# Kernel optimization log

Hardware: AMD Instinct MI355X
Metric: run time of the kernel (lower is better)

The kernel has to match this reference:

```python
import jax, jax.numpy as jnp
import numpy as np

B, S, IN, E, L, H, NC, NL = 4, 1000, 5, 256, 6, 8, 2, 50
DH = E // H


def _ln(x, g, b, eps=1e-5):
    m = jnp.mean(x, -1, keepdims=True)
    v = jnp.mean((x - m) ** 2, -1, keepdims=True)
    return (x - m) / jnp.sqrt(v + eps) * g + b


def _lin(x, w, b):
    return x @ w.T + b


def _ph_single(points, fw, db, law, lab):
    # points: (S, 2) -> (6,) persistence features
    scores = (points @ law.T + lab)[:, 0]
    wts = jax.nn.softmax(scores)
    _, idx = jax.lax.top_k(wts, NL)
    lm = points[idx]  # (NL, 2) landmarks
    d2 = jnp.sum((lm[:, None, :] - lm[None, :, :]) ** 2, -1)
    # safe sqrt (zero grad on zero diagonal) == torch.cdist
    dist = jnp.sqrt(jnp.where(d2 > 0, d2, 1.0)) * (d2 > 0)
    sd = dist * jnp.abs(fw[0, 0]) + db[0]
    K = jnp.exp(-sd)
    lap = jnp.diag(jnp.sum(K, 1)) - K
    ev, evec = jnp.linalg.eigh(lap)
    zm = (ev < 1e-6).astype(ev.dtype)
    n0 = jnp.sum(zm)
    s0 = jnp.sum(jnp.abs(ev) * zm)
    gap = ev[1] - ev[0]
    fied = jnp.std(evec[:, 1], ddof=1)  # torch.std is unbiased
    return jnp.stack([n0, s0, gap, fied, jnp.mean(ev[2:6]), jnp.std(ev[2:6], ddof=1)])


def _attn(x, pf, qw, qb, kw, kb, vw, vb, pw1, pb1, pw2, pb2, ow_, ob_):
    b, s, e = x.shape
    q = _lin(x, qw, qb).reshape(b, s, H, DH).transpose(0, 2, 1, 3)
    k = _lin(x, kw, kb).reshape(b, s, H, DH).transpose(0, 2, 1, 3)
    v = _lin(x, vw, vb).reshape(b, s, H, DH).transpose(0, 2, 1, 3)
    scores = jnp.einsum('bhqd,bhkd->bhqk', q, k) / DH ** 0.5
    tw = jax.nn.sigmoid(_lin(jax.nn.relu(_lin(pf, pw1, pb1)), pw2, pb2))  # (b, E)
    # expand + mean over embed dim collapses to one scalar per sample
    ts = jnp.mean(tw, -1).reshape(b, 1, 1, 1)
    aw = jax.nn.softmax(scores * ts, -1)
    out = jnp.einsum('bhqk,bhkd->bhqd', aw, v).transpose(0, 2, 1, 3).reshape(b, s, e)
    return _lin(out, ow_, ob_)


def _fwd(sequences, ph_fw, ph_db, ph_law, ph_lab,
         emb_w1, emb_b1, emb_w2, emb_b2, emb_ln_g, emb_ln_b, pos_enc,
         qw, qb, kw, kb, vw, vb, pe_w1, pe_b1, pe_w2, pe_b2, ow, ob,
         ln_g, ln_b, f_w1, f_b1, f_w2, f_b2,
         c_ln_g, c_ln_b, c_w1, c_b1, c_w2, c_b2):
    b, s, _ = sequences.shape
    t = jnp.broadcast_to(jnp.arange(s, dtype=sequences.dtype), (b, s))
    pc = jnp.stack([t, jnp.mean(sequences, 2)], 2)  # (b, s, 2) point clouds
    pf = jax.vmap(lambda p: _ph_single(p, ph_fw, ph_db, ph_law, ph_lab))(pc)  # (b, 6)
    x = _ln(_lin(jax.nn.relu(_lin(sequences, emb_w1, emb_b1)), emb_w2, emb_b2),
            emb_ln_g, emb_ln_b)
    x = x + pos_enc[:s][None]
    for l in range(L):
        att = _attn(x, pf, qw[l], qb[l], kw[l], kb[l], vw[l], vb[l],
                    pe_w1[l], pe_b1[l], pe_w2[l], pe_b2[l], ow[l], ob[l])
        x = _ln(x + att, ln_g[l], ln_b[l])  # NOTE: same LN reused twice, as in source
        ff = _lin(jax.nn.gelu(_lin(x, f_w1[l], f_b1[l]), approximate=False), f_w2[l], f_b2[l])
        x = _ln(x + ff, ln_g[l], ln_b[l])
    pwts = jax.nn.softmax(jnp.sum(x, -1), -1)[..., None]
    pooled = jnp.sum(x * pwts, 1)
    z = jax.nn.relu(_lin(_ln(pooled, c_ln_g, c_ln_b), c_w1, c_b1))
    return _lin(z, c_w2, c_b2)


def setup_inputs() -> dict:
    key = jax.random.key(0)
    ks = iter(jax.random.split(key, 64))

    def w(shape, fan_in):
        return jax.random.normal(next(ks), shape, jnp.float32) / np.sqrt(fan_in).astype(np.float32)

    z = lambda *sh: jnp.zeros(sh, jnp.float32)
    o = lambda *sh: jnp.ones(sh, jnp.float32)
    return dict(
        sequences=jax.random.normal(next(ks), (B, S, IN), jnp.float32),
        ph_fw=jnp.full((1, 1), 0.02, jnp.float32),  # small filtration scale keeps eigh well-conditioned
        ph_db=z(1),
        ph_law=w((1, 2), 2), ph_lab=z(1),
        emb_w1=w((E // 2, IN), IN), emb_b1=z(E // 2),
        emb_w2=w((E, E // 2), E // 2), emb_b2=z(E),
        emb_ln_g=o(E), emb_ln_b=z(E),
        pos_enc=jax.random.normal(next(ks), (1000, E), jnp.float32),
        qw=w((L, E, E), E), qb=z(L, E),
        kw=w((L, E, E), E), kb=z(L, E),
        vw=w((L, E, E), E), vb=z(L, E),
        pe_w1=w((L, E // 2, 6), 6), pe_b1=z(L, E // 2),
        pe_w2=w((L, E, E // 2), E // 2), pe_b2=z(L, E),
        ow=w((L, E, E), E), ob=z(L, E),
        ln_g=o(L, E), ln_b=z(L, E),
        f_w1=w((L, 4 * E, E), E), f_b1=z(L, 4 * E),
        f_w2=w((L, E, 4 * E), 4 * E), f_b2=z(L, E),
        c_ln_g=o(E), c_ln_b=z(E),
        c_w1=w((E // 2, E), E), c_b1=z(E // 2),
        c_w2=w((NC, E // 2), E // 2), c_b2=z(NC),
    )


def reference(sequences, ph_fw, ph_db, ph_law, ph_lab,
              emb_w1, emb_b1, emb_w2, emb_b2, emb_ln_g, emb_ln_b, pos_enc,
              qw, qb, kw, kb, vw, vb, pe_w1, pe_b1, pe_w2, pe_b2, ow, ob,
              ln_g, ln_b, f_w1, f_b1, f_w2, f_b2,
              c_ln_g, c_ln_b, c_w1, c_b1, c_w2, c_b2):
    return _fwd(sequences, ph_fw, ph_db, ph_law, ph_lab,
                emb_w1, emb_b1, emb_w2, emb_b2, emb_ln_g, emb_ln_b, pos_enc,
                qw, qb, kw, kb, vw, vb, pe_w1, pe_b1, pe_w2, pe_b2, ow, ob,
                ln_g, ln_b, f_w1, f_b1, f_w2, f_b2,
                c_ln_g, c_ln_b, c_w1, c_b1, c_w2, c_b2)
```

## Files before the change

### kernel.cpp

```cpp
#include <hip/hip_runtime.h>
#include <math.h>

constexpr int BB = 4;
constexpr int SS = 1000;
constexpr int INDIM = 5;
constexpr int EE = 256;
constexpr int LL = 6;
constexpr int HH = 8;
constexpr int DHH = 32;
constexpr int NLM = 50;
constexpr int FFD = 1024;

typedef short short8 __attribute__((ext_vector_type(8)));
typedef float f32x4 __attribute__((ext_vector_type(4)));
typedef unsigned short u16;
typedef unsigned long long u64;

__device__ inline u16 f2b(float f) {
  union { float f; unsigned u; } v; v.f = f;
  unsigned u = v.u;
  unsigned r = u + 0x7FFFu + ((u >> 16) & 1u);
  return (u16)(r >> 16);
}
__device__ inline float b2f(u16 b) {
  union { unsigned u; float f; } v; v.u = ((unsigned)b) << 16;
  return v.f;
}
__device__ inline short8 pack8(float4 a, float4 b) {
  short8 r;
  r[0] = (short)f2b(a.x); r[1] = (short)f2b(a.y);
  r[2] = (short)f2b(a.z); r[3] = (short)f2b(a.w);
  r[4] = (short)f2b(b.x); r[5] = (short)f2b(b.y);
  r[6] = (short)f2b(b.z); r[7] = (short)f2b(b.w);
  return r;
}

__device__ inline double wred_sum(double v) {
#pragma unroll
  for (int m = 1; m < 64; m <<= 1) v += __shfl_xor(v, m, 64);
  return v;
}
__device__ inline double wred_min(double v) {
#pragma unroll
  for (int m = 1; m < 64; m <<= 1) v = fmin(v, __shfl_xor(v, m, 64));
  return v;
}
__device__ inline double wred_max(double v) {
#pragma unroll
  for (int m = 1; m < 64; m <<= 1) v = fmax(v, __shfl_xor(v, m, 64));
  return v;
}
__device__ inline float wredf_sum(float v) {
#pragma unroll
  for (int m = 1; m < 64; m <<= 1) v += __shfl_xor(v, m, 64);
  return v;
}
__device__ inline int sgnbit(double x) {
  return (int)((unsigned long long)__double_as_longlong(x) >> 63);
}
__device__ inline u64 shflx64(u64 v, int m) {
  unsigned lo = (unsigned)v, hi = (unsigned)(v >> 32);
  lo = __shfl_xor(lo, m, 64);
  hi = __shfl_xor(hi, m, 64);
  return ((u64)hi << 32) | lo;
}

struct PhS {
  union {
    double matA[NLM][51];
    double vstore[NLM - 2][64];
  } u;
  double vbuf[104];
  double vw[208];
  double dar[NLM], ear[NLM], e2a[NLM], tauA[NLM], evs[NLM];
  double gdl[NLM], gdd[NLM], gdu[NLM], gdu2[NLM], gz[NLM];
  float sm[SS];
  float lx[NLM], ly[NLM];
};
struct EmS { float h[128]; };
union FusedS { PhS ph; EmS em; };

__global__ __launch_bounds__(64, 1) void phembed_kernel(
    const float* __restrict__ seq, const float* __restrict__ ph_fw,
    const float* __restrict__ ph_db, const float* __restrict__ ph_law,
    const float* __restrict__ ph_lab, float* __restrict__ pf,
    const float* __restrict__ ew1, const float* __restrict__ eb1,
    const float* __restrict__ ew2, const float* __restrict__ eb2,
    const float* __restrict__ eg, const float* __restrict__ ebe,
    const float* __restrict__ pos, float* __restrict__ X)
{
  __shared__ FusedS S;
  const int lane = threadIdx.x;

  if (blockIdx.x < BB) {
    const int b = blockIdx.x;
    PhS& P = S.ph;
    const float law0 = ph_law[0], law1 = ph_law[1], labv = ph_lab[0];

    u64 key[16];
#pragma unroll
    for (int r = 0; r < 16; ++r) {
      int s = lane * 16 + r;
      u64 k;
      if (s < SS) {
        const float* p = seq + ((size_t)b * SS + s) * INDIM;
        float m = (p[0] + p[1] + p[2] + p[3] + p[4]) * 0.2f;
        P.sm[s] = m;
        float sc = (float)s * law0 + m * law1 + labv;
        unsigned u = __float_as_uint(sc);
        unsigned asc = (u & 0x80000000u) ? ~u : (u | 0x80000000u);
        k = ((u64)(~asc) << 32) | (unsigned)s;
      } else {
        k = (0xFFFFFFFFull << 32) | (unsigned)s;
      }
      key[r] = k;
    }
#pragma unroll
    for (int k = 2; k <= 1024; k <<= 1) {
#pragma unroll
      for (int j = 512; j > 0; j >>= 1) {
        if (j > k / 2) continue;
        if (j >= 16) {
          const int lx = j >> 4;
          const bool lowerL = ((lane & lx) == 0);
          const bool upL = (((lane << 4) & k) == 0);
          const bool keepmin = (lowerL == upL);
#pragma unroll
          for (int r = 0; r < 16; ++r) {
            u64 p = shflx64(key[r], lx);
            bool take = keepmin ? (p < key[r]) : (p > key[r]);
            key[r] = take ? p : key[r];
          }
        } else {
#pragma unroll
          for (int r = 0; r < 16; ++r) {
            const int r2 = r ^ j;
            if (r2 > r) {
              int i = (lane << 4) | r;
              bool up = ((i & k) == 0);
              u64 a = key[r], c = key[r2];
              if ((a > c) == up) { key[r] = c; key[r2] = a; }
            }
          }
        }
      }
    }
    __builtin_amdgcn_wave_barrier();
#pragma unroll
    for (int r = 0; r < 16; ++r) {
      int i = lane * 16 + r;
      if (i < NLM) {
        int id = (int)(key[r] & 0xFFFFFFFFull);
        P.lx[i] = (float)id;
        P.ly[i] = P.sm[id];
      }
    }
    __builtin_amdgcn_wave_barrier();
    const float fwv = fabsf(ph_fw[0]);
    const float dbv = ph_db[0];
    for (int t = lane; t < NLM * NLM; t += 64) {
      int i = t / NLM, j = t % NLM;
      float dx = P.lx[i] - P.lx[j], dy = P.ly[i] - P.ly[j];
      float d2 = dx * dx + dy * dy;
      float dist = (d2 > 0.f) ? sqrtf(d2) : 0.f;
      float Kv = expf(-(dist * fwv + dbv));
      P.u.matA[i][j] = -(double)Kv;
    }
    __builtin_amdgcn_wave_barrier();
    if (lane < NLM) {
      double rsum = 0.0;
      for (int j = 0; j < NLM; ++j) rsum -= P.u.matA[lane][j];
      P.u.matA[lane][lane] += rsum;
    }
    for (int t = lane; t < 104; t += 64) {
      P.vbuf[t] = 0.0; P.vw[2 * t] = 0.0; P.vw[2 * t + 1] = 0.0;
    }
    __builtin_amdgcn_wave_barrier();

    double rrow[NLM];
#pragma unroll
    for (int j = 0; j < NLM; ++j)
      rrow[j] = (lane < NLM) ? P.u.matA[lane][j] : 0.0;
    double dval = 0.0;
    __builtin_amdgcn_wave_barrier();

    for (int k = 0; k <= NLM - 3; ++k) {
      if (lane == k) dval = rrow[0];
      double x = (lane > k && lane < NLM) ? rrow[0] : 0.0;
      double x0 = __shfl(x, k + 1, 64);
      double sigma = wred_sum((lane > k + 1) ? x * x : 0.0);
      double beta, tau, scale;
      if (sigma == 0.0) { beta = x0; tau = 0.0; scale = 0.0; }
      else {
        double nrm = sqrt(x0 * x0 + sigma);
        beta = (x0 >= 0.0) ? -nrm : nrm;
        tau = (beta - x0) / beta;
        scale = 1.0 / (x0 - beta);
      }
      double v = (lane == k + 1) ? 1.0 : ((lane > k + 1) ? x * scale : 0.0);
      P.vbuf[lane] = v;
      P.vw[2 * lane] = v;
      P.u.vstore[k][lane] = v;
      if (lane == 0) { P.ear[k] = beta; P.tauA[k] = tau; }
      __builtin_amdgcn_wave_barrier();
      double a0 = 0.0, a1 = 0.0, a2 = 0.0, a3 = 0.0;
#pragma unroll
      for (int j = 1; j < NLM; j += 4) {
        a0 += rrow[j] * P.vbuf[k + j];
        if (j + 1 < NLM) a1 += rrow[j + 1] * P.vbuf[k + j + 1];
        if (j + 2 < NLM) a2 += rrow[j + 2] * P.vbuf[k + j + 2];
        if (j + 3 < NLM) a3 += rrow[j + 3] * P.vbuf[k + j + 3];
      }
      double p = ((a0 + a1) + (a2 + a3)) * tau;
      double dotvp = wred_sum(v * p);
      double w = p - 0.5 * tau * dotvp * v;
      P.vw[2 * lane + 1] = w;
      __builtin_amdgcn_wave_barrier();
#pragma unroll
      for (int j = 1; j < NLM; ++j) {
        double vj = P.vw[2 * (k + j)], wj = P.vw[2 * (k + j) + 1];
        rrow[j] -= v * wj + w * vj;
      }
      __builtin_amdgcn_wave_barrier();
#pragma unroll
      for (int j = 0; j < NLM - 1; ++j) rrow[j] = rrow[j + 1];
      rrow[NLM - 1] = 0.0;
    }
    {
      double d48 = __shfl(rrow[0], NLM - 2, 64);
      double e48 = __shfl(rrow[1], NLM - 2, 64);
      double d49 = __shfl(rrow[1], NLM - 1, 64);
      if (lane == NLM - 2) dval = d48;
      if (lane == NLM - 1) dval = d49;
      if (lane == 0) P.ear[NLM - 2] = e48;
      if (lane < NLM) P.dar[lane] = dval;
      __builtin_amdgcn_wave_barrier();
      if (lane < NLM - 1) P.e2a[lane] = P.ear[lane] * P.ear[lane];
      __builtin_amdgcn_wave_barrier();
    }

    double lo_i = 1e300, hi_i = -1e300;
    if (lane < NLM) {
      double rl = (lane > 0) ? fabs(P.ear[lane - 1]) : 0.0;
      double rr = (lane < NLM - 1) ? fabs(P.ear[lane]) : 0.0;
      double dd = P.dar[lane];
      lo_i = dd - rl - rr;
      hi_i = dd + rl + rr;
    }
    double glo = wred_min(lo_i), ghi = wred_max(hi_i);

    double myev = 1e300;
    if (lane < NLM) {
      double lo = glo, hi = ghi;
      const int need = lane + 1;
      for (int it = 0; it < 24; ++it) {
        double third = (hi - lo) * (1.0 / 3.0);
        double x1 = lo + third, x2 = hi - third;
        double pA = P.dar[0] - x1, pB = P.dar[0] - x2;
        double qA = 1.0, qB = 1.0;
        int c1 = sgnbit(pA), c2 = sgnbit(pB);
#pragma unroll 7
        for (int i = 1; i < NLM; ++i) {
          double di = P.dar[i], ei = P.e2a[i - 1];
          double nA = (di - x1) * pA - ei * qA;
          double nB = (di - x2) * pB - ei * qB;
          if (nA == 0.0) nA = sgnbit(pA) ? -1e-300 : 1e-300;
          if (nB == 0.0) nB = sgnbit(pB) ? -1e-300 : 1e-300;
          c1 += (sgnbit(nA) != sgnbit(pA));
          c2 += (sgnbit(nB) != sgnbit(pB));
          long long aa = __double_as_longlong(nA) & 0x7fffffffffffffffLL;
          long long ap = __double_as_longlong(pA) & 0x7fffffffffffffffLL;
          int Ea = (int)((aa > ap ? aa : ap) >> 52);
          int sea = 2046 - Ea; sea = sea < 1 ? 1 : (sea > 2045 ? 2045 : sea);
          double sA = __longlong_as_double((long long)sea << 52);
          qA = pA * sA; pA = nA * sA;
          long long ab = __double_as_longlong(nB) & 0x7fffffffffffffffLL;
          long long ab2 = __double_as_longlong(pB) & 0x7fffffffffffffffLL;
          int Eb = (int)((ab > ab2 ? ab : ab2) >> 52);
          int seb = 2046 - Eb; seb = seb < 1 ? 1 : (seb > 2045 ? 2045 : seb);
          double sB = __longlong_as_double((long long)seb << 52);
          qB = pB * sB; pB = nB * sB;
        }
        if (c1 >= need) hi = x1;
        else if (c2 >= need) { lo = x1; hi = x2; }
        else lo = x2;
      }
      myev = 0.5 * (lo + hi);
      P.evs[lane] = myev;
    }
    __builtin_amdgcn_wave_barrier();

    if (lane == 0) {
      double shift = P.evs[1];
      unsigned rs = 12345u;
      for (int i = 0; i < NLM; ++i) {
        rs = rs * 1103515245u + 12345u;
        P.gz[i] = ((double)((rs >> 8) & 0xFFFF)) / 65536.0 - 0.5;
      }
      for (int iter = 0; iter < 2; ++iter) {
        for (int i = 0; i < NLM; ++i) P.gdd[i] = P.dar[i] - shift;
        for (int i = 0; i < NLM - 1; ++i) { P.gdl[i] = P.ear[i]; P.gdu[i] = P.ear[i]; }
        for (int i = 0; i < NLM - 1; ++i) {
          if (fabs(P.gdd[i]) >= fabs(P.gdl[i])) {
            if (P.gdd[i] == 0.0) P.gdd[i] = 1e-280;
            double fact = P.gdl[i] / P.gdd[i];
            P.gdd[i + 1] -= fact * P.gdu[i];
            P.gz[i + 1] -= fact * P.gz[i];
            if (i < NLM - 2) P.gdu2[i] = 0.0;
          } else {
            double fact = P.gdd[i] / P.gdl[i];
            P.gdd[i] = P.gdl[i];
            double tmp = P.gdd[i + 1];
            P.gdd[i + 1] = P.gdu[i] - fact * tmp;
            if (i < NLM - 2) { P.gdu2[i] = P.gdu[i + 1]; P.gdu[i + 1] = -fact * P.gdu2[i]; }
            P.gdu[i] = tmp;
            double tz = P.gz[i]; P.gz[i] = P.gz[i + 1]; P.gz[i + 1] = tz - fact * P.gz[i];
          }
        }
        if (P.gdd[NLM - 1] == 0.0) P.gdd[NLM - 1] = 1e-280;
        P.gz[NLM - 1] /= P.gdd[NLM - 1];
        P.gz[NLM - 2] = (P.gz[NLM - 2] - P.gdu[NLM - 2] * P.gz[NLM - 1]) / P.gdd[NLM - 2];
        for (int i = NLM - 3; i >= 0; --i)
          P.gz[i] = (P.gz[i] - P.gdu[i] * P.gz[i + 1] - P.gdu2[i] * P.gz[i + 2]) / P.gdd[i];
        double nr = 0.0;
        for (int i = 0; i < NLM; ++i) nr += P.gz[i] * P.gz[i];
        nr = sqrt(nr);
        for (int i = 0; i < NLM; ++i) P.gz[i] /= nr;
      }
    }
    __builtin_amdgcn_wave_barrier();
    double fied = (lane < NLM) ? P.gz[lane] : 0.0;
    for (int k = NLM - 3; k >= 0; --k) {
      double v = P.u.vstore[k][lane];
      double dot = wred_sum(v * fied);
      fied -= P.tauA[k] * dot * v;
    }

    bool inR = (lane < NLM);
    double n0 = wred_sum((inR && myev < 1e-6) ? 1.0 : 0.0);
    double s0 = wred_sum((inR && myev < 1e-6) ? fabs(myev) : 0.0);
    double e0 = __shfl(myev, 0, 64), e1 = __shfl(myev, 1, 64);
    double e2 = __shfl(myev, 2, 64), e3 = __shfl(myev, 3, 64);
    double e4 = __shfl(myev, 4, 64), e5 = __shfl(myev, 5, 64);
    double gap = e1 - e0;
    double m4 = (e2 + e3 + e4 + e5) * 0.25;
    double v4 = ((e2 - m4) * (e2 - m4) + (e3 - m4) * (e3 - m4) +
                 (e4 - m4) * (e4 - m4) + (e5 - m4) * (e5 - m4)) / 3.0;
    double fmean = wred_sum(inR ? fied : 0.0) / NLM;
    double fd = inR ? (fied - fmean) : 0.0;
    double fvar = wred_sum(fd * fd) / (NLM - 1);
    if (lane == 0) {
      float* o = pf + b * 6;
      o[0] = (float)n0;
      o[1] = (float)s0;
      o[2] = (float)gap;
      o[3] = (float)sqrt(fvar);
      o[4] = (float)m4;
      o[5] = (float)sqrt(v4);
    }
    return;
  }

  const int row = blockIdx.x - BB;
  const int s = row % SS;
  EmS& M2 = S.em;
  float sv0, sv1, sv2, sv3, sv4;
  {
    const float* p = seq + (size_t)row * INDIM;
    sv0 = p[0]; sv1 = p[1]; sv2 = p[2]; sv3 = p[3]; sv4 = p[4];
  }
#pragma unroll
  for (int half = 0; half < 2; ++half) {
    int j = lane + half * 64;
    const float* w = ew1 + j * INDIM;
    float a = eb1[j] + w[0] * sv0 + w[1] * sv1 + w[2] * sv2 + w[3] * sv3 + w[4] * sv4;
    M2.h[j] = fmaxf(a, 0.f);
  }
  __builtin_amdgcn_wave_barrier();
  float o4[4];
#pragma unroll
  for (int q = 0; q < 4; ++q) {
    int e = lane * 4 + q;
    const float* w = ew2 + (size_t)e * 128;
    float a0 = 0.f, a1 = 0.f;
    for (int i = 0; i < 128; i += 8) {
      float4 wa = *(const float4*)(w + i);
      float4 wb = *(const float4*)(w + i + 4);
      a0 += wa.x * M2.h[i] + wa.y * M2.h[i + 1] + wa.z * M2.h[i + 2] + wa.w * M2.h[i + 3];
      a1 += wb.x * M2.h[i + 4] + wb.y * M2.h[i + 5] + wb.z * M2.h[i + 6] + wb.w * M2.h[i + 7];
    }
    o4[q] = eb2[e] + a0 + a1;
  }
  float ssum = o4[0] + o4[1] + o4[2] + o4[3];
  ssum = wredf_sum(ssum);
  float mean = ssum * (1.f / EE);
  float d0 = o4[0] - mean, d1 = o4[1] - mean, d2 = o4[2] - mean, d3 = o4[3] - mean;
  float qsum = d0 * d0 + d1 * d1 + d2 * d2 + d3 * d3;
  qsum = wredf_sum(qsum);
  float inv = rsqrtf(qsum * (1.f / EE) + 1e-5f);
  float4 gv = *(const float4*)(eg + lane * 4);
  float4 bv = *(const float4*)(ebe + lane * 4);
  float4 pv = *(const float4*)(pos + (size_t)s * EE + lane * 4);
  float4 outv = make_float4(d0 * inv * gv.x + bv.x + pv.x,
                            d1 * inv * gv.y + bv.y + pv.y,
                            d2 * inv * gv.z + bv.z + pv.z,
                            d3 * inv * gv.w + bv.w + pv.w);
  *(float4*)(X + (size_t)row * EE + lane * 4) = outv;
}

__global__ __launch_bounds__(256) void temp_kernel(
    const float* __restrict__ pf, const float* __restrict__ w1, const float* __restrict__ b1,
    const float* __restrict__ w2, const float* __restrict__ b2, float* __restrict__ ts)
{
  const int l = blockIdx.x / BB, b = blockIdx.x % BB, tid = threadIdx.x;
  __shared__ float pfl[6];
  __shared__ float h[128];
  __shared__ float red[256];
  if (tid < 6) pfl[tid] = pf[b * 6 + tid];
  __syncthreads();
  if (tid < 128) {
    const float* w = w1 + ((size_t)l * 128 + tid) * 6;
    float a = b1[(size_t)l * 128 + tid];
#pragma unroll
    for (int i = 0; i < 6; ++i) a += w[i] * pfl[i];
    h[tid] = fmaxf(a, 0.f);
  }
  __syncthreads();
  const float* w = w2 + ((size_t)l * EE + tid) * 128;
  float a = b2[(size_t)l * EE + tid];
  for (int i = 0; i < 128; ++i) a += w[i] * h[i];
  float sg = 1.f / (1.f + expf(-a));
  red[tid] = sg; __syncthreads();
  for (int wd = 128; wd > 0; wd >>= 1) { if (tid < wd) red[tid] += red[tid + wd]; __syncthreads(); }
  if (tid == 0) ts[l * BB + b] = red[0] * (1.f / EE);
}

template <int AF32, int ACT>
__global__ __launch_bounds__(256) void gemm_bt(
    const void* __restrict__ Aptr,
    const float* __restrict__ W0, const float* __restrict__ W1, const float* __restrict__ W2,
    const float* __restrict__ bb0, const float* __restrict__ bb1, const float* __restrict__ bb2,
    u16* __restrict__ C0, u16* __restrict__ C1, u16* __restrict__ C2,
    int M, int N, int K)
{
  const int z = blockIdx.z;
  const float* W = (z == 0) ? W0 : (z == 1) ? W1 : W2;
  const float* bias = (z == 0) ? bb0 : (z == 1) ? bb1 : bb2;
  u16* C = (z == 0) ? C0 : (z == 1) ? C1 : C2;
  __shared__ __align__(16) u16 As[2][64][40];
  __shared__ __align__(16) u16 Bs[2][64][40];
  const int m0 = blockIdx.x * 64, n0 = blockIdx.y * 64;
  const int tid = threadIdx.x;
  const int lane = tid & 63, wave = tid >> 6;
  const int wm = wave >> 1, wn = wave & 1;
  const int l15 = lane & 15, l4 = lane >> 4;
  const int srow = tid >> 2, scg = (tid & 3) * 8;

  const float* Af = (const float*)Aptr;
  const u16* Ab = (const u16*)Aptr;

  f32x4 acc[2][2];
#pragma unroll
  for (int i = 0; i < 2; ++i)
#pragma unroll
    for (int j = 0; j < 2; ++j) acc[i][j] = (f32x4){0.f, 0.f, 0.f, 0.f};

  short8 areg, breg;
  auto do_load = [&](int t) {
    int kk = t * 32 + scg;
    if (AF32) {
      float4 a0 = *(const float4*)(Af + (size_t)(m0 + srow) * K + kk);
      float4 a1 = *(const float4*)(Af + (size_t)(m0 + srow) * K + kk + 4);
      areg = pack8(a0, a1);
    } else {
      areg = *(const short8*)(Ab + (size_t)(m0 + srow) * K + kk);
    }
    float4 b0 = *(const float4*)(W + (size_t)(n0 + srow) * K + kk);
    float4 b1 = *(const float4*)(W + (size_t)(n0 + srow) * K + kk + 4);
    breg = pack8(b0, b1);
  };
  auto do_write = [&](int buf) {
    *(short8*)&As[buf][srow][scg] = areg;
    *(short8*)&Bs[buf][srow][scg] = breg;
  };

  const int NT = K / 32;
  do_load(0);
  do_write(0);
  __syncthreads();
  for (int t = 0; t < NT; ++t) {
    const int cur = t & 1;
    if (t + 1 < NT) do_load(t + 1);
    short8 af0 = *(const short8*)&As[cur][wm * 32 + l15][l4 * 8];
    short8 af1 = *(const short8*)&As[cur][wm * 32 + 16 + l15][l4 * 8];
    short8 bf0 = *(const short8*)&Bs[cur][wn * 32 + l15][l4 * 8];
    short8 bf1 = *(const short8*)&Bs[cur][wn * 32 + 16 + l15][l4 * 8];
    acc[0][0] = __builtin_amdgcn_mfma_f32_16x16x32_bf16(af0, bf0, acc[0][0], 0, 0, 0);
    acc[0][1] = __builtin_amdgcn_mfma_f32_16x16x32_bf16(af0, bf1, acc[0][1], 0, 0, 0);
    acc[1][0] = __builtin_amdgcn_mfma_f32_16x16x32_bf16(af1, bf0, acc[1][0], 0, 0, 0);
    acc[1][1] = __builtin_amdgcn_mfma_f32_16x16x32_bf16(af1, bf1, acc[1][1], 0, 0, 0);
    if (t + 1 < NT) do_write(cur ^ 1);
    __syncthreads();
  }
#pragma unroll
  for (int nf = 0; nf < 2; ++nf) {
    int col = n0 + wn * 32 + nf * 16 + l15;
    float bv = bias[col];
#pragma unroll
    for (int mf = 0; mf < 2; ++mf) {
#pragma unroll
      for (int r = 0; r < 4; ++r) {
        int row = m0 + wm * 32 + mf * 16 + l4 * 4 + r;
        if (row < M) {
          float v = acc[mf][nf][r] + bv;
          if (ACT == 1) v = 0.5f * v * (1.f + erff(v * 0.70710678118654752440f));
          C[(size_t)row * N + col] = f2b(v);
        }
      }
    }
  }
}

__global__ __launch_bounds__(256) void attn_mfma(
    const u16* __restrict__ Qm, const u16* __restrict__ Km, const u16* __restrict__ Vm,
    const float* __restrict__ ts, u16* __restrict__ Om, int l)
{
  const int qt = blockIdx.x, h = blockIdx.y, b = blockIdx.z;
  const int tid = threadIdx.x;
  const int lane = tid & 63, wave = tid >> 6;
  const int l15 = lane & 15, l4 = lane >> 4;
  const float scale = ts[l * BB + b] * 0.17677669529663688110f;
  __shared__ __align__(16) u16 Ks[64][40];
  __shared__ __align__(16) u16 Vt[32][72];
  __shared__ __align__(16) u16 Pw[4][16][72];
  const int q0 = qt * 64 + wave * 16;
  const int srow = tid >> 2, scg = (tid & 3) * 8;

  short8 qf = {0, 0, 0, 0, 0, 0, 0, 0};
  {
    int qrow = q0 + l15;
    if (qrow < SS)
      qf = *(const short8*)(Qm + ((size_t)(b * SS + qrow)) * EE + h * DHH + l4 * 8);
  }

  float mrun[4] = {-INFINITY, -INFINITY, -INFINITY, -INFINITY};
  float lrun[4] = {0.f, 0.f, 0.f, 0.f};
  f32x4 Oacc[2];
  Oacc[0] = (f32x4){0.f, 0.f, 0.f, 0.f};
  Oacc[1] = (f32x4){0.f, 0.f, 0.f, 0.f};

  for (int k0 = 0; k0 < SS; k0 += 64) {
    int kn = SS - k0; if (kn > 64) kn = 64;
    __syncthreads();
    {
      short8 kv8 = {0, 0, 0, 0, 0, 0, 0, 0};
      if (srow < kn)
        kv8 = *(const short8*)(Km + ((size_t)(b * SS + k0 + srow)) * EE + h * DHH + scg);
      *(short8*)&Ks[srow][scg] = kv8;
    }
    {
      int d = tid & 31, kb = tid >> 5;
      u16 uu[8];
#pragma unroll
      for (int i = 0; i < 8; ++i) {
        int kv = kb * 8 + i;
        uu[i] = (kv < kn) ? Vm[((size_t)(b * SS + k0 + kv)) * EE + h * DHH + d] : (u16)0;
      }
      *(ushort4*)(&Vt[d][kb * 8])     = make_ushort4(uu[0], uu[1], uu[2], uu[3]);
      *(ushort4*)(&Vt[d][kb * 8 + 4]) = make_ushort4(uu[4], uu[5], uu[6], uu[7]);
    }
    __syncthreads();

    f32x4 sa[4];
#pragma unroll
    for (int nf = 0; nf < 4; ++nf) {
      short8 kf = *(const short8*)(&Ks[nf * 16 + l15][l4 * 8]);
      f32x4 zz = (f32x4){0.f, 0.f, 0.f, 0.f};
      sa[nf] = __builtin_amdgcn_mfma_f32_16x16x32_bf16(qf, kf, zz, 0, 0, 0);
    }
#pragma unroll
    for (int nf = 0; nf < 4; ++nf) {
      bool valid = (nf * 16 + l15) < kn;
#pragma unroll
      for (int r = 0; r < 4; ++r)
        sa[nf][r] = valid ? sa[nf][r] * scale : -INFINITY;
    }
    float pv[4][4];
#pragma unroll
    for (int r = 0; r < 4; ++r) {
      float tmax = fmaxf(fmaxf(sa[0][r], sa[1][r]), fmaxf(sa[2][r], sa[3][r]));
#pragma unroll
      for (int m = 1; m < 16; m <<= 1) tmax = fmaxf(tmax, __shfl_xor(tmax, m, 64));
      float mnew = fmaxf(mrun[r], tmax);
      float fac = expf(mrun[r] - mnew);
      float rsum = 0.f;
#pragma unroll
      for (int nf = 0; nf < 4; ++nf) {
        float p = expf(sa[nf][r] - mnew);
        pv[nf][r] = p;
        rsum += p;
      }
#pragma unroll
      for (int m = 1; m < 16; m <<= 1) rsum += __shfl_xor(rsum, m, 64);
      lrun[r] = lrun[r] * fac + rsum;
      mrun[r] = mnew;
      Oacc[0][r] *= fac;
      Oacc[1][r] *= fac;
    }
#pragma unroll
    for (int nf = 0; nf < 4; ++nf)
#pragma unroll
      for (int r = 0; r < 4; ++r)
        Pw[wave][l4 * 4 + r][nf * 16 + l15] = f2b(pv[nf][r]);
    asm volatile("s_waitcnt lgkmcnt(0)" ::: "memory");
    __builtin_amdgcn_sched_barrier(0);
#pragma unroll
    for (int ka = 0; ka < 2; ++ka) {
      short8 pa = *(const short8*)(&Pw[wave][l15][ka * 32 + l4 * 8]);
#pragma unroll
      for (int df = 0; df < 2; ++df) {
        short8 vf = *(const short8*)(&Vt[df * 16 + l15][ka * 32 + l4 * 8]);
        Oacc[df] = __builtin_amdgcn_mfma_f32_16x16x32_bf16(pa, vf, Oacc[df], 0, 0, 0);
      }
    }
  }
#pragma unroll
  for (int df = 0; df < 2; ++df)
#pragma unroll
    for (int r = 0; r < 4; ++r) {
      int qrow = q0 + l4 * 4 + r;
      if (qrow < SS)
        Om[((size_t)(b * SS + qrow)) * EE + h * DHH + df * 16 + l15] = f2b(Oacc[df][r] / lrun[r]);
    }
}

__global__ __launch_bounds__(256) void addln_kernel(
    float* __restrict__ X, const u16* __restrict__ T,
    const float* __restrict__ g, const float* __restrict__ be)
{
  const int row = blockIdx.x * 4 + (threadIdx.x >> 6);
  const int lane = threadIdx.x & 63;
  float4 xv = *(float4*)(X + (size_t)row * EE + lane * 4);
  ushort4 tv = *(const ushort4*)(T + (size_t)row * EE + lane * 4);
  float4 v = make_float4(xv.x + b2f(tv.x), xv.y + b2f(tv.y),
                         xv.z + b2f(tv.z), xv.w + b2f(tv.w));
  float s = v.x + v.y + v.z + v.w;
  s = wredf_sum(s);
  float mean = s * (1.f / EE);
  float4 d = make_float4(v.x - mean, v.y - mean, v.z - mean, v.w - mean);
  float q = d.x * d.x + d.y * d.y + d.z * d.z + d.w * d.w;
  q = wredf_sum(q);
  float inv = rsqrtf(q * (1.f / EE) + 1e-5f);
  float4 gv = *(const float4*)(g + lane * 4);
  float4 bv = *(const float4*)(be + lane * 4);
  float4 o = make_float4(d.x * inv * gv.x + bv.x, d.y * inv * gv.y + bv.y,
                         d.z * inv * gv.z + bv.z, d.w * inv * gv.w + bv.w);
  *(float4*)(X + (size_t)row * EE + lane * 4) = o;
}

__global__ __launch_bounds__(256) void final_kernel(
    const float* __restrict__ X, const float* __restrict__ g, const float* __restrict__ be,
    const float* __restrict__ w1, const float* __restrict__ b1,
    const float* __restrict__ w2, const float* __restrict__ b2,
    float* __restrict__ out)
{
  const int b = blockIdx.x, tid = threadIdx.x;
  __shared__ float rs[SS];
  __shared__ float red[256];
  __shared__ float pooled[EE];
  __shared__ float h[128];
  for (int s = tid; s < SS; s += 256) {
    const float* xr = X + ((size_t)(b * SS + s)) * EE;
    float a = 0.f;
    for (int e = 0; e < EE; ++e) a += xr[e];
    rs[s] = a;
  }
  __syncthreads();
  float mx = -INFINITY;
  for (int s = tid; s < SS; s += 256) mx = fmaxf(mx, rs[s]);
  red[tid] = mx; __syncthreads();
  for (int w = 128; w > 0; w >>= 1) { if (tid < w) red[tid] = fmaxf(red[tid], red[tid + w]); __syncthreads(); }
  mx = red[0]; __syncthreads();
  float sme = 0.f;
  for (int s = tid; s < SS; s += 256) { float e2 = expf(rs[s] - mx); rs[s] = e2; sme += e2; }
  red[tid] = sme; __syncthreads();
  for (int w = 128; w > 0; w >>= 1) { if (tid < w) red[tid] += red[tid + w]; __syncthreads(); }
  float tot = red[0]; __syncthreads();
  float acc = 0.f;
  for (int s = 0; s < SS; ++s) acc += X[((size_t)(b * SS + s)) * EE + tid] * rs[s];
  acc /= tot;
  red[tid] = acc; __syncthreads();
  for (int w = 128; w > 0; w >>= 1) { if (tid < w) red[tid] += red[tid + w]; __syncthreads(); }
  float mean = red[0] * (1.f / EE); __syncthreads();
  float d = acc - mean;
  red[tid] = d * d; __syncthreads();
  for (int w = 128; w > 0; w >>= 1) { if (tid < w) red[tid] += red[tid + w]; __syncthreads(); }
  float var = red[0] * (1.f / EE);
  pooled[tid] = d * rsqrtf(var + 1e-5f) * g[tid] + be[tid];
  __syncthreads();
  if (tid < 128) {
    const float* w = w1 + (size_t)tid * EE;
    float a = b1[tid];
    for (int e = 0; e < EE; ++e) a += w[e] * pooled[e];
    h[tid] = fmaxf(a, 0.f);
  }
  __syncthreads();
  if (tid < 2) {
    const float* w = w2 + (size_t)tid * 128;
    float a = b2[tid];
    for (int j = 0; j < 128; ++j) a += w[j] * h[j];
    out[b * 2 + tid] = a;
  }
}

extern "C" void kernel_launch(void* const* d_in, const int* in_sizes, int n_in,
                              void* d_out, int out_size, void* d_ws, size_t ws_size,
                              hipStream_t stream) {
  (void)in_sizes; (void)n_in; (void)out_size; (void)ws_size;
  const float* seq    = (const float*)d_in[0];
  const float* ph_fw  = (const float*)d_in[1];
  const float* ph_db  = (const float*)d_in[2];
  const float* ph_law = (const float*)d_in[3];
  const float* ph_lab = (const float*)d_in[4];
  const float* emb_w1 = (const float*)d_in[5];
  const float* emb_b1 = (const float*)d_in[6];
  const float* emb_w2 = (const float*)d_in[7];
  const float* emb_b2 = (const float*)d_in[8];
  const float* eln_g  = (const float*)d_in[9];
  const float* eln_b  = (const float*)d_in[10];
  const float* pos    = (const float*)d_in[11];
  const float* qw     = (const float*)d_in[12];
  const float* qb     = (const float*)d_in[13];
  const float* kw     = (const float*)d_in[14];
  const float* kb     = (const float*)d_in[15];
  const float* vw     = (const float*)d_in[16];
  const float* vb     = (const float*)d_in[17];
  const float* pw1    = (const float*)d_in[18];
  const float* pb1    = (const float*)d_in[19];
  const float* pw2    = (const float*)d_in[20];
  const float* pb2    = (const float*)d_in[21];
  const float* ow     = (const float*)d_in[22];
  const float* obv    = (const float*)d_in[23];
  const float* lng    = (const float*)d_in[24];
  const float* lnb    = (const float*)d_in[25];
  const float* fw1    = (const float*)d_in[26];
  const float* fb1    = (const float*)d_in[27];
  const float* fw2    = (const float*)d_in[28];
  const float* fb2    = (const float*)d_in[29];
  const float* clng   = (const float*)d_in[30];
  const float* clnb   = (const float*)d_in[31];
  const float* cw1    = (const float*)d_in[32];
  const float* cb1    = (const float*)d_in[33];
  const float* cw2    = (const float*)d_in[34];
  const float* cb2    = (const float*)d_in[35];

  float* ws  = (float*)d_ws;
  float* pf  = ws;
  float* tsv = ws + 32;
  const size_t SL = (size_t)4096 * 256;
  float* X = ws + 256;
  u16* Qb   = (u16*)(X + SL);
  u16* Kb   = Qb + SL;
  u16* Vb   = Kb + SL;
  u16* ATTb = Vb + SL;
  u16* TMPb = ATTb + SL;
  u16* HIDb = TMPb + SL;
  const int M = BB * SS;

  phembed_kernel<<<BB + M, 64, 0, stream>>>(
      seq, ph_fw, ph_db, ph_law, ph_lab, pf,
      emb_w1, emb_b1, emb_w2, emb_b2, eln_g, eln_b, pos, X);
  temp_kernel<<<LL * BB, 256, 0, stream>>>(pf, pw1, pb1, pw2, pb2, tsv);

  const int GM = 63;
  for (int l = 0; l < LL; ++l) {
    const size_t wo = (size_t)l * EE * EE;
    gemm_bt<1, 0><<<dim3(GM, EE / 64, 3), 256, 0, stream>>>(
        X, qw + wo, kw + wo, vw + wo, qb + l * EE, kb + l * EE, vb + l * EE,
        Qb, Kb, Vb, M, EE, EE);
    attn_mfma<<<dim3(16, HH, BB), 256, 0, stream>>>(Qb, Kb, Vb, tsv, ATTb, l);
    gemm_bt<0, 0><<<dim3(GM, EE / 64, 1), 256, 0, stream>>>(
        ATTb, ow + wo, ow + wo, ow + wo, obv + l * EE, obv + l * EE, obv + l * EE,
        TMPb, TMPb, TMPb, M, EE, EE);
    addln_kernel<<<M / 4, 256, 0, stream>>>(X, TMPb, lng + l * EE, lnb + l * EE);
    gemm_bt<1, 1><<<dim3(GM, FFD / 64, 1), 256, 0, stream>>>(
        X, fw1 + (size_t)l * FFD * EE, fw1 + (size_t)l * FFD * EE, fw1 + (size_t)l * FFD * EE,
        fb1 + (size_t)l * FFD, fb1 + (size_t)l * FFD, fb1 + (size_t)l * FFD,
        HIDb, HIDb, HIDb, M, FFD, EE);
    gemm_bt<0, 0><<<dim3(GM, EE / 64, 1), 256, 0, stream>>>(
        HIDb, fw2 + (size_t)l * EE * FFD, fw2 + (size_t)l * EE * FFD, fw2 + (size_t)l * EE * FFD,
        fb2 + l * EE, fb2 + l * EE, fb2 + l * EE,
        TMPb, TMPb, TMPb, M, EE, FFD);
    addln_kernel<<<M / 4, 256, 0, stream>>>(X, TMPb, lng + l * EE, lnb + l * EE);
  }

  final_kernel<<<BB, 256, 0, stream>>>(X, clng, clnb, cw1, cb1, cw2, cb2, (float*)d_out);
}
```

Baseline: 1.032 ms.

## Spread persistence-homology block across four waves and pack embedding rows per block

The PH block now runs with 256 threads. The bitonic sort moves to shared memory, and the Householder tridiagonalisation splits its matvec and rank-2 update across four waves, keeping the matrix in LDS instead of registers. Sturm bisection gives each trisection point its own lane. Embedding blocks now process four rows each with 256 threads, cutting the block count. In exchange, the serial PH chain gains many block-wide barriers and LDS traffic in place of register-resident data.

```diff
diff --git a/kernel.cpp b/kernel.cpp
--- a/kernel.cpp
+++ b/kernel.cpp
@@ -58,29 +58,23 @@
 __device__ inline int sgnbit(double x) {
   return (int)((unsigned long long)__double_as_longlong(x) >> 63);
 }
-__device__ inline u64 shflx64(u64 v, int m) {
-  unsigned lo = (unsigned)v, hi = (unsigned)(v >> 32);
-  lo = __shfl_xor(lo, m, 64);
-  hi = __shfl_xor(hi, m, 64);
-  return ((u64)hi << 32) | lo;
-}
 
 struct PhS {
+  double matA[NLM][51];
   union {
-    double matA[NLM][51];
+    u64 keys[1024];
     double vstore[NLM - 2][64];
   } u;
-  double vbuf[104];
-  double vw[208];
+  double vbuf[64], wbuf[64];
+  double pm[4][64];
   double dar[NLM], ear[NLM], e2a[NLM], tauA[NLM], evs[NLM];
   double gdl[NLM], gdd[NLM], gdu[NLM], gdu2[NLM], gz[NLM];
   float sm[SS];
   float lx[NLM], ly[NLM];
 };
-struct EmS { float h[128]; };
-union FusedS { PhS ph; EmS em; };
-
-__global__ __launch_bounds__(64, 1) void phembed_kernel(
+union FusedS { PhS ph; float h[4][128]; };
+
+__global__ __launch_bounds__(256) void phembed_kernel(
     const float* __restrict__ seq, const float* __restrict__ ph_fw,
     const float* __restrict__ ph_db, const float* __restrict__ ph_law,
     const float* __restrict__ ph_lab, float* __restrict__ pf,
@@ -90,18 +84,15 @@
     const float* __restrict__ pos, float* __restrict__ X)
 {
   __shared__ FusedS S;
-  const int lane = threadIdx.x;
+  const int tid = threadIdx.x;
+  const int lane = tid & 63, wid = tid >> 6;
 
   if (blockIdx.x < BB) {
     const int b = blockIdx.x;
     PhS& P = S.ph;
     const float law0 = ph_law[0], law1 = ph_law[1], labv = ph_lab[0];
-
-    u64 key[16];
-#pragma unroll
-    for (int r = 0; r < 16; ++r) {
-      int s = lane * 16 + r;
-      u64 k;
+    for (int s = tid; s < 1024; s += 256) {
+      u64 key;
       if (s < SS) {
         const float* p = seq + ((size_t)b * SS + s) * INDIM;
         float m = (p[0] + p[1] + p[2] + p[3] + p[4]) * 0.2f;
@@ -109,135 +100,109 @@
         float sc = (float)s * law0 + m * law1 + labv;
         unsigned u = __float_as_uint(sc);
         unsigned asc = (u & 0x80000000u) ? ~u : (u | 0x80000000u);
-        k = ((u64)(~asc) << 32) | (unsigned)s;
+        key = ((u64)(~asc) << 32) | (unsigned)s;
       } else {
-        k = (0xFFFFFFFFull << 32) | (unsigned)s;
-      }
-      key[r] = k;
-    }
-#pragma unroll
+        key = (0xFFFFFFFFull << 32) | (unsigned)s;
+      }
+      P.u.keys[s] = key;
+    }
+    __syncthreads();
     for (int k = 2; k <= 1024; k <<= 1) {
-#pragma unroll
-      for (int j = 512; j > 0; j >>= 1) {
-        if (j > k / 2) continue;
-        if (j >= 16) {
-          const int lx = j >> 4;
-          const bool lowerL = ((lane & lx) == 0);
-          const bool upL = (((lane << 4) & k) == 0);
-          const bool keepmin = (lowerL == upL);
-#pragma unroll
-          for (int r = 0; r < 16; ++r) {
-            u64 p = shflx64(key[r], lx);
-            bool take = keepmin ? (p < key[r]) : (p > key[r]);
-            key[r] = take ? p : key[r];
-          }
-        } else {
-#pragma unroll
-          for (int r = 0; r < 16; ++r) {
-            const int r2 = r ^ j;
-            if (r2 > r) {
-              int i = (lane << 4) | r;
-              bool up = ((i & k) == 0);
-              u64 a = key[r], c = key[r2];
-              if ((a > c) == up) { key[r] = c; key[r2] = a; }
-            }
+      for (int j = k >> 1; j > 0; j >>= 1) {
+        for (int i = tid; i < 1024; i += 256) {
+          int ixj = i ^ j;
+          if (ixj > i) {
+            u64 a = P.u.keys[i], c = P.u.keys[ixj];
+            bool up = ((i & k) == 0);
+            if ((a > c) == up) { P.u.keys[i] = c; P.u.keys[ixj] = a; }
           }
         }
-      }
-    }
-    __builtin_amdgcn_wave_barrier();
-#pragma unroll
-    for (int r = 0; r < 16; ++r) {
-      int i = lane * 16 + r;
-      if (i < NLM) {
-        int id = (int)(key[r] & 0xFFFFFFFFull);
-        P.lx[i] = (float)id;
-        P.ly[i] = P.sm[id];
-      }
-    }
-    __builtin_amdgcn_wave_barrier();
+        __syncthreads();
+      }
+    }
+    if (tid < NLM) {
+      int id = (int)(P.u.keys[tid] & 0xFFFFFFFFull);
+      P.lx[tid] = (float)id;
+      P.ly[tid] = P.sm[id];
+    }
+    __syncthreads();
     const float fwv = fabsf(ph_fw[0]);
     const float dbv = ph_db[0];
-    for (int t = lane; t < NLM * NLM; t += 64) {
+    for (int t = tid; t < NLM * NLM; t += 256) {
       int i = t / NLM, j = t % NLM;
       float dx = P.lx[i] - P.lx[j], dy = P.ly[i] - P.ly[j];
       float d2 = dx * dx + dy * dy;
       float dist = (d2 > 0.f) ? sqrtf(d2) : 0.f;
       float Kv = expf(-(dist * fwv + dbv));
-      P.u.matA[i][j] = -(double)Kv;
-    }
-    __builtin_amdgcn_wave_barrier();
-    if (lane < NLM) {
+      P.matA[i][j] = -(double)Kv;
+    }
+    __syncthreads();
+    if (tid < NLM) {
       double rsum = 0.0;
-      for (int j = 0; j < NLM; ++j) rsum -= P.u.matA[lane][j];
-      P.u.matA[lane][lane] += rsum;
-    }
-    for (int t = lane; t < 104; t += 64) {
-      P.vbuf[t] = 0.0; P.vw[2 * t] = 0.0; P.vw[2 * t + 1] = 0.0;
-    }
-    __builtin_amdgcn_wave_barrier();
-
-    double rrow[NLM];
-#pragma unroll
-    for (int j = 0; j < NLM; ++j)
-      rrow[j] = (lane < NLM) ? P.u.matA[lane][j] : 0.0;
-    double dval = 0.0;
-    __builtin_amdgcn_wave_barrier();
+      for (int j = 0; j < NLM; ++j) rsum -= P.matA[tid][j];
+      P.matA[tid][tid] += rsum;
+    }
+    __syncthreads();
 
     for (int k = 0; k <= NLM - 3; ++k) {
-      if (lane == k) dval = rrow[0];
-      double x = (lane > k && lane < NLM) ? rrow[0] : 0.0;
-      double x0 = __shfl(x, k + 1, 64);
-      double sigma = wred_sum((lane > k + 1) ? x * x : 0.0);
-      double beta, tau, scale;
-      if (sigma == 0.0) { beta = x0; tau = 0.0; scale = 0.0; }
-      else {
-        double nrm = sqrt(x0 * x0 + sigma);
-        beta = (x0 >= 0.0) ? -nrm : nrm;
-        tau = (beta - x0) / beta;
-        scale = 1.0 / (x0 - beta);
-      }
-      double v = (lane == k + 1) ? 1.0 : ((lane > k + 1) ? x * scale : 0.0);
-      P.vbuf[lane] = v;
-      P.vw[2 * lane] = v;
-      P.u.vstore[k][lane] = v;
-      if (lane == 0) { P.ear[k] = beta; P.tauA[k] = tau; }
-      __builtin_amdgcn_wave_barrier();
-      double a0 = 0.0, a1 = 0.0, a2 = 0.0, a3 = 0.0;
-#pragma unroll
-      for (int j = 1; j < NLM; j += 4) {
-        a0 += rrow[j] * P.vbuf[k + j];
-        if (j + 1 < NLM) a1 += rrow[j + 1] * P.vbuf[k + j + 1];
-        if (j + 2 < NLM) a2 += rrow[j + 2] * P.vbuf[k + j + 2];
-        if (j + 3 < NLM) a3 += rrow[j + 3] * P.vbuf[k + j + 3];
-      }
-      double p = ((a0 + a1) + (a2 + a3)) * tau;
-      double dotvp = wred_sum(v * p);
-      double w = p - 0.5 * tau * dotvp * v;
-      P.vw[2 * lane + 1] = w;
-      __builtin_amdgcn_wave_barrier();
-#pragma unroll
-      for (int j = 1; j < NLM; ++j) {
-        double vj = P.vw[2 * (k + j)], wj = P.vw[2 * (k + j) + 1];
-        rrow[j] -= v * wj + w * vj;
-      }
-      __builtin_amdgcn_wave_barrier();
-#pragma unroll
-      for (int j = 0; j < NLM - 1; ++j) rrow[j] = rrow[j + 1];
-      rrow[NLM - 1] = 0.0;
-    }
-    {
-      double d48 = __shfl(rrow[0], NLM - 2, 64);
-      double e48 = __shfl(rrow[1], NLM - 2, 64);
-      double d49 = __shfl(rrow[1], NLM - 1, 64);
-      if (lane == NLM - 2) dval = d48;
-      if (lane == NLM - 1) dval = d49;
-      if (lane == 0) P.ear[NLM - 2] = e48;
-      if (lane < NLM) P.dar[lane] = dval;
-      __builtin_amdgcn_wave_barrier();
-      if (lane < NLM - 1) P.e2a[lane] = P.ear[lane] * P.ear[lane];
-      __builtin_amdgcn_wave_barrier();
-    }
+      if (wid == 0) {
+        double x = (lane > k && lane < NLM) ? P.matA[lane][k] : 0.0;
+        double x0 = __shfl(x, k + 1, 64);
+        double sigma = wred_sum((lane > k + 1) ? x * x : 0.0);
+        double beta, tau, scale;
+        if (sigma == 0.0) { beta = x0; tau = 0.0; scale = 0.0; }
+        else {
+          double nrm = sqrt(x0 * x0 + sigma);
+          beta = (x0 >= 0.0) ? -nrm : nrm;
+          tau = (beta - x0) / beta;
+          scale = 1.0 / (x0 - beta);
+        }
+        double v = (lane == k + 1) ? 1.0 : ((lane > k + 1 && lane < NLM) ? x * scale : 0.0);
+        P.vbuf[lane] = v;
+        P.u.vstore[k][lane] = v;
+        if (lane == 0) { P.ear[k] = beta; P.tauA[k] = tau; }
+      }
+      __syncthreads();
+      {
+        double partial = 0.0;
+        if (lane < NLM) {
+          int j0 = wid * 13;
+#pragma unroll
+          for (int jj = 0; jj < 13; ++jj) {
+            int j = j0 + jj;
+            if (j < NLM) partial += P.matA[lane][j] * P.vbuf[j];
+          }
+        }
+        P.pm[wid][lane] = partial;
+      }
+      __syncthreads();
+      if (wid == 0) {
+        double tau = P.tauA[k];
+        double p = 0.0;
+        if (lane < NLM)
+          p = (P.pm[0][lane] + P.pm[1][lane] + P.pm[2][lane] + P.pm[3][lane]) * tau;
+        double vr = P.vbuf[lane];
+        double dotvp = wred_sum(vr * p);
+        double w = p - 0.5 * tau * dotvp * vr;
+        P.wbuf[lane] = (lane < NLM) ? w : 0.0;
+      }
+      __syncthreads();
+      if (lane < NLM) {
+        double vr = P.vbuf[lane], wr = P.wbuf[lane];
+        int j0 = wid * 13;
+#pragma unroll
+        for (int jj = 0; jj < 13; ++jj) {
+          int j = j0 + jj;
+          if (j < NLM) P.matA[lane][j] -= vr * P.wbuf[j] + wr * P.vbuf[j];
+        }
+      }
+      __syncthreads();
+    }
+    if (tid < NLM) P.dar[tid] = P.matA[tid][tid];
+    if (tid == 0) P.ear[NLM - 2] = P.matA[NLM - 1][NLM - 2];
+    __syncthreads();
+    if (tid < NLM - 1) P.e2a[tid] = P.ear[tid] * P.ear[tid];
+    __syncthreads();
 
     double lo_i = 1e300, hi_i = -1e300;
     if (lane < NLM) {
@@ -249,46 +214,41 @@
     }
     double glo = wred_min(lo_i), ghi = wred_max(hi_i);
 
-    double myev = 1e300;
-    if (lane < NLM) {
+    if (tid < 100) {
+      const int e = tid >> 1;
+      const int side = tid & 1;
+      const int need = e + 1;
       double lo = glo, hi = ghi;
-      const int need = lane + 1;
       for (int it = 0; it < 24; ++it) {
         double third = (hi - lo) * (1.0 / 3.0);
         double x1 = lo + third, x2 = hi - third;
-        double pA = P.dar[0] - x1, pB = P.dar[0] - x2;
-        double qA = 1.0, qB = 1.0;
-        int c1 = sgnbit(pA), c2 = sgnbit(pB);
+        double x = side ? x2 : x1;
+        double p = P.dar[0] - x, q = 1.0;
+        int c = sgnbit(p);
 #pragma unroll 7
         for (int i = 1; i < NLM; ++i) {
-          double di = P.dar[i], ei = P.e2a[i - 1];
-          double nA = (di - x1) * pA - ei * qA;
-          double nB = (di - x2) * pB - ei * qB;
-          if (nA == 0.0) nA = sgnbit(pA) ? -1e-300 : 1e-300;
-          if (nB == 0.0) nB = sgnbit(pB) ? -1e-300 : 1e-300;
-          c1 += (sgnbit(nA) != sgnbit(pA));
-          c2 += (sgnbit(nB) != sgnbit(pB));
-          long long aa = __double_as_longlong(nA) & 0x7fffffffffffffffLL;
-          long long ap = __double_as_longlong(pA) & 0x7fffffffffffffffLL;
-          int Ea = (int)((aa > ap ? aa : ap) >> 52);
-          int sea = 2046 - Ea; sea = sea < 1 ? 1 : (sea > 2045 ? 2045 : sea);
-          double sA = __longlong_as_double((long long)sea << 52);
-          qA = pA * sA; pA = nA * sA;
-          long long ab = __double_as_longlong(nB) & 0x7fffffffffffffffLL;
-          long long ab2 = __double_as_longlong(pB) & 0x7fffffffffffffffLL;
-          int Eb = (int)((ab > ab2 ? ab : ab2) >> 52);
-          int seb = 2046 - Eb; seb = seb < 1 ? 1 : (seb > 2045 ? 2045 : seb);
-          double sB = __longlong_as_double((long long)seb << 52);
-          qB = pB * sB; pB = nB * sB;
+          double n = (P.dar[i] - x) * p - P.e2a[i - 1] * q;
+          if (n == 0.0) n = sgnbit(p) ? -1e-300 : 1e-300;
+          c += (sgnbit(n) != sgnbit(p));
+          long long an = __double_as_longlong(n) & 0x7fffffffffffffffLL;
+          long long ap = __double_as_longlong(p) & 0x7fffffffffffffffLL;
+          int E = (int)((an > ap ? an : ap) >> 52);
+          int se = 2046 - E; se = se < 1 ? 1 : (se > 2045 ? 2045 : se);
+          double s = __longlong_as_double((long long)se << 52);
+          q = p * s; p = n * s;
         }
+        int cp = __shfl_xor(c, 1, 64);
+        int c1 = side ? cp : c;
+        int c2 = side ? c : cp;
         if (c1 >= need) hi = x1;
         else if (c2 >= need) { lo = x1; hi = x2; }
         else lo = x2;
       }
-      myev = 0.5 * (lo + hi);
-      P.evs[lane] = myev;
-    }
-    __builtin_amdgcn_wave_barrier();
+      if (side == 0) P.evs[e] = 0.5 * (lo + hi);
+    }
+    __syncthreads();
+
+    if (wid != 0) return;
 
     if (lane == 0) {
       double shift = P.evs[1];
@@ -336,12 +296,12 @@
       fied -= P.tauA[k] * dot * v;
     }
 
+    double myev = (lane < NLM) ? P.evs[lane] : 1e300;
     bool inR = (lane < NLM);
     double n0 = wred_sum((inR && myev < 1e-6) ? 1.0 : 0.0);
     double s0 = wred_sum((inR && myev < 1e-6) ? fabs(myev) : 0.0);
-    double e0 = __shfl(myev, 0, 64), e1 = __shfl(myev, 1, 64);
-    double e2 = __shfl(myev, 2, 64), e3 = __shfl(myev, 3, 64);
-    double e4 = __shfl(myev, 4, 64), e5 = __shfl(myev, 5, 64);
+    double e0 = P.evs[0], e1 = P.evs[1];
+    double e2 = P.evs[2], e3 = P.evs[3], e4 = P.evs[4], e5 = P.evs[5];
     double gap = e1 - e0;
     double m4 = (e2 + e3 + e4 + e5) * 0.25;
     double v4 = ((e2 - m4) * (e2 - m4) + (e3 - m4) * (e3 - m4) +
@@ -361,9 +321,9 @@
     return;
   }
 
-  const int row = blockIdx.x - BB;
+  const int row = (blockIdx.x - BB) * 4 + wid;
   const int s = row % SS;
-  EmS& M2 = S.em;
+  float* hb = S.h[wid];
   float sv0, sv1, sv2, sv3, sv4;
   {
     const float* p = seq + (size_t)row * INDIM;
@@ -374,7 +334,7 @@
     int j = lane + half * 64;
     const float* w = ew1 + j * INDIM;
     float a = eb1[j] + w[0] * sv0 + w[1] * sv1 + w[2] * sv2 + w[3] * sv3 + w[4] * sv4;
-    M2.h[j] = fmaxf(a, 0.f);
+    hb[j] = fmaxf(a, 0.f);
   }
   __builtin_amdgcn_wave_barrier();
   float o4[4];
@@ -386,8 +346,8 @@
     for (int i = 0; i < 128; i += 8) {
       float4 wa = *(const float4*)(w + i);
       float4 wb = *(const float4*)(w + i + 4);
-      a0 += wa.x * M2.h[i] + wa.y * M2.h[i + 1] + wa.z * M2.h[i + 2] + wa.w * M2.h[i + 3];
-      a1 += wb.x * M2.h[i + 4] + wb.y * M2.h[i + 5] + wb.z * M2.h[i + 6] + wb.w * M2.h[i + 7];
+      a0 += wa.x * hb[i] + wa.y * hb[i + 1] + wa.z * hb[i + 2] + wa.w * hb[i + 3];
+      a1 += wb.x * hb[i + 4] + wb.y * hb[i + 5] + wb.z * hb[i + 6] + wb.w * hb[i + 7];
     }
     o4[q] = eb2[e] + a0 + a1;
   }
@@ -767,7 +727,7 @@
   u16* HIDb = TMPb + SL;
   const int M = BB * SS;
 
-  phembed_kernel<<<BB + M, 64, 0, stream>>>(
+  phembed_kernel<<<BB + M / 4, 256, 0, stream>>>(
       seq, ph_fw, ph_db, ph_law, ph_lab, pf,
       emb_w1, emb_b1, emb_w2, emb_b2, eln_g, eln_b, pos, X);
   temp_kernel<<<LL * BB, 256, 0, stream>>>(pf, pw1, pb1, pw2, pb2, tsv);
```

After: 979.4 us. 5.1% less time.
